# Optimization experiments

Measured on AMD Instinct MI355X. Metric: run time of the kernel, lower is better.

The kernel has to match this reference:

```python
import jax, jax.numpy as jnp
import numpy as np

LOCAL_K = 3
TOKEN_T, TOKEN_H, TOKEN_W = 8, 32, 32  # N = T*H*W = 8192
HIDDEN, N_HEADS = 256, 8


def _gather_neighbors(kv):
    # kv: [B, N, D2] -> [B, N, 27, D2] of 3x3x3 neighborhood (zero padded)
    B, N, D2 = kv.shape
    pad = LOCAL_K // 2
    x3d = kv.reshape(B, TOKEN_T, TOKEN_H, TOKEN_W, D2)
    x3d = jnp.pad(x3d, ((0, 0), (pad, pad), (pad, pad), (pad, pad), (0, 0)))
    slices = [
        x3d[:, dt:dt + TOKEN_T, dh:dh + TOKEN_H, dw:dw + TOKEN_W, :]
        for dt in range(LOCAL_K)
        for dh in range(LOCAL_K)
        for dw in range(LOCAL_K)
    ]
    nb = jnp.stack(slices, axis=4)  # [B, T, H, W, 27, D2]
    return nb.reshape(B, N, LOCAL_K ** 3, D2)


def setup_inputs() -> dict:
    key = jax.random.key(0)
    k1, k2, k3 = jax.random.split(key, 3)
    B, N, D = 2, TOKEN_T * TOKEN_H * TOKEN_W, HIDDEN
    x = jax.random.normal(k1, (B, N, D), dtype=jnp.float32)
    w_qkv = jax.random.normal(k2, (3 * D, D), dtype=jnp.float32) * (D ** -0.5)
    w_out = jax.random.normal(k3, (D, D), dtype=jnp.float32) * (D ** -0.5)
    return {"x": x, "w_qkv": w_qkv, "w_out": w_out}


def reference(x, w_qkv, w_out):
    B, N, D = x.shape
    H, d = N_HEADS, D // N_HEADS
    qkv = x @ w_qkv.T                       # [B, N, 3D]
    q, k, v = jnp.split(qkv, 3, axis=-1)
    kv_nb = _gather_neighbors(jnp.concatenate([k, v], axis=-1))  # [B,N,27,2D]
    k_nb, v_nb = jnp.split(kv_nb, 2, axis=-1)
    q = q.reshape(B, N, H, d)
    k_nb = k_nb.reshape(B, N, 27, H, d)
    v_nb = v_nb.reshape(B, N, 27, H, d)
    scale = 1.0 / jnp.sqrt(jnp.asarray(d, dtype=q.dtype))
    scores = jnp.einsum('bnhd,bnkhd->bnhk', q, k_nb) * scale  # [B,N,H,27]
    attn = jax.nn.softmax(scores, axis=-1)
    out = jnp.einsum('bnhk,bnkhd->bnhd', attn, v_nb)           # [B,N,H,d]
    return out.reshape(B, N, D) @ w_out.T
```

## Files before the change

kernel.cpp:

```cpp
#include <hip/hip_runtime.h>
#include <hip/hip_bf16.h>

#define TOK_T 8
#define TOK_H 32
#define TOK_W 32
#define NTOK 8192
#define BATCH 2
#define DMODEL 256
#define D3 768
#define NHEADS 8
#define DHEAD 32

using short8  = __attribute__((ext_vector_type(8))) short;
using ushort8 = __attribute__((ext_vector_type(8))) unsigned short;
using f32x4   = __attribute__((ext_vector_type(4))) float;
using f32x2   = __attribute__((ext_vector_type(2))) float;

__device__ __forceinline__ ushort f2bf(float f) {
  __hip_bfloat16 h = __float2bfloat16(f);
  return *reinterpret_cast<ushort*>(&h);
}
__device__ __forceinline__ float bf2f(ushort u) {
  union { unsigned u; float f; } v; v.u = ((unsigned)u) << 16;
  return v.f;
}
__device__ __forceinline__ f32x2 bfpair(unsigned u) {
  union { unsigned u; float f; } lo, hi;
  lo.u = u << 16;
  hi.u = u & 0xffff0000u;
  f32x2 r; r[0] = lo.f; r[1] = hi.f;
  return r;
}

template<int TBM, int TBN, int NW, int NBN, bool AF32, bool OUTBF16>
__global__ __launch_bounds__(NW * 64, 4) void gemm_fused(const void* __restrict__ Av,
                                                         const float* __restrict__ B,
                                                         void* __restrict__ Cv,
                                                         int ldc) {
  constexpr int NCW = TBN / 64;
  constexpr int NWR = NW / NCW;
  constexpr int MR  = TBM / (NWR * 16);
  constexpr int CHA = TBM * 4;
  constexpr int CHB = TBN * 4;
  constexpr int NT  = NW * 64;
  constexpr int CPT = (CHA + CHB) / NT;
  constexpr int SA  = CHA / NT;
  constexpr int ATILE = TBM * 32;
  constexpr int BTILE = TBN * 32;

  __shared__ __align__(16) ushort sm[2][ATILE + BTILE];

  const int tid  = threadIdx.x;
  const int lane = tid & 63;
  const int wid  = tid >> 6;
  const int wr   = wid / NCW;
  const int wc   = wid % NCW;
  const int bid  = blockIdx.x;
  const int xcd  = bid & 7;
  const int kk2  = bid >> 3;
  const int bm   = ((kk2 / NBN) * 8 + xcd) * TBM;
  const int bn   = (kk2 % NBN) * TBN;
  const int fr   = lane & 15;
  const int kb   = lane >> 4;

  float4  laf[SA > 0 ? SA : 1][2];
  ushort8 lab[SA > 0 ? SA : 1];
  float4  lbf[CPT - SA][2];

  auto load = [&](int kt) {
#pragma unroll
    for (int s = 0; s < SA; ++s) {
      int cc = tid + s * NT;
      int r = cc >> 2, sl = cc & 3;
      if constexpr (AF32) {
        const float* p = (const float*)Av + (size_t)(bm + r) * 256 + kt + sl * 8;
        laf[s][0] = *(const float4*)p;
        laf[s][1] = *(const float4*)(p + 4);
      } else {
        lab[s] = *(const ushort8*)((const ushort*)Av + (size_t)(bm + r) * 256 + kt + sl * 8);
      }
    }
#pragma unroll
    for (int s = 0; s < CPT - SA; ++s) {
      int cc = tid + (s + SA) * NT - CHA;
      int r = cc >> 2, sl = cc & 3;
      const float* p = B + (size_t)(bn + r) * 256 + kt + sl * 8;
      lbf[s][0] = *(const float4*)p;
      lbf[s][1] = *(const float4*)(p + 4);
    }
  };
  auto stow = [&](int buf) {
#pragma unroll
    for (int s = 0; s < SA; ++s) {
      int cc = tid + s * NT;
      int r = cc >> 2, sl = cc & 3;
      int sck = r * 4 + (sl ^ ((r >> 1) & 3));
      ushort8 v;
      if constexpr (AF32) {
        v[0] = f2bf(laf[s][0].x); v[1] = f2bf(laf[s][0].y);
        v[2] = f2bf(laf[s][0].z); v[3] = f2bf(laf[s][0].w);
        v[4] = f2bf(laf[s][1].x); v[5] = f2bf(laf[s][1].y);
        v[6] = f2bf(laf[s][1].z); v[7] = f2bf(laf[s][1].w);
      } else v = lab[s];
      *(ushort8*)&sm[buf][sck * 8] = v;
    }
#pragma unroll
    for (int s = 0; s < CPT - SA; ++s) {
      int cc = tid + (s + SA) * NT - CHA;
      int r = cc >> 2, sl = cc & 3;
      int sck = r * 4 + (sl ^ ((r >> 1) & 3));
      ushort8 v;
      v[0] = f2bf(lbf[s][0].x); v[1] = f2bf(lbf[s][0].y);
      v[2] = f2bf(lbf[s][0].z); v[3] = f2bf(lbf[s][0].w);
      v[4] = f2bf(lbf[s][1].x); v[5] = f2bf(lbf[s][1].y);
      v[6] = f2bf(lbf[s][1].z); v[7] = f2bf(lbf[s][1].w);
      *(ushort8*)&sm[buf][ATILE + sck * 8] = v;
    }
  };

  f32x4 acc[MR][4] = {};

  load(0);
  stow(0);
  __syncthreads();

  for (int it = 0; it < 8; ++it) {
    const int cur = it & 1;
    if (it < 7) load((it + 1) * 32);

    short8 af[MR], bf8[4];
#pragma unroll
    for (int m = 0; m < MR; ++m) {
      int r  = wr * (MR * 16) + m * 16 + fr;
      int ck = r * 4 + (kb ^ ((r >> 1) & 3));
      af[m] = *(const short8*)&sm[cur][ck * 8];
    }
#pragma unroll
    for (int n = 0; n < 4; ++n) {
      int r  = wc * 64 + n * 16 + fr;
      int ck = r * 4 + (kb ^ ((r >> 1) & 3));
      bf8[n] = *(const short8*)&sm[cur][ATILE + ck * 8];
    }
#pragma unroll
    for (int m = 0; m < MR; ++m)
#pragma unroll
      for (int n = 0; n < 4; ++n)
        acc[m][n] = __builtin_amdgcn_mfma_f32_16x16x32_bf16(af[m], bf8[n], acc[m][n], 0, 0, 0);

    if (it < 7) {
      stow(cur ^ 1);
      __syncthreads();
    }
  }

  if constexpr (OUTBF16) {
    ushort* C = (ushort*)Cv;
#pragma unroll
    for (int m = 0; m < MR; ++m)
#pragma unroll
      for (int n = 0; n < 4; ++n)
#pragma unroll
        for (int j = 0; j < 4; ++j) {
          int row = bm + wr * (MR * 16) + m * 16 + kb * 4 + j;
          int col = bn + wc * 64 + n * 16 + fr;
          C[(size_t)row * ldc + col] = f2bf(acc[m][n][j]);
        }
  } else {
    float* C = (float*)Cv;
#pragma unroll
    for (int m = 0; m < MR; ++m)
#pragma unroll
      for (int n = 0; n < 4; ++n)
#pragma unroll
        for (int j = 0; j < 4; ++j) {
          int row = bm + wr * (MR * 16) + m * 16 + kb * 4 + j;
          int col = bn + wc * 64 + n * 16 + fr;
          C[(size_t)row * ldc + col] = acc[m][n][j];
        }
  }
}

#define HALO 600

__global__ __launch_bounds__(256, 2) void local_attn(const ushort* __restrict__ qkv,
                                                     ushort* __restrict__ aob) {
  __shared__ __align__(16) ushort sh[HALO * 64];
  const int tile = blockIdx.x;
  const int head = blockIdx.y;
  const int b    = blockIdx.z;
  const int tz = tile >> 4;
  const int ty = (tile >> 2) & 3;
  const int tx = tile & 3;
  const int t0 = tz * 4, h0 = ty * 8, w0 = tx * 8;
  const int tid = threadIdx.x;

  for (int idx = tid; idx < HALO; idx += 256) {
    int ht  = idx / 100;
    int rem = idx - ht * 100;
    int hh  = rem / 10;
    int hw  = rem - hh * 10;
    int gt = t0 - 1 + ht, gh = h0 - 1 + hh, gw = w0 - 1 + hw;
    ushort* row = &sh[idx * 64];
    const int sw = idx & 7;
    if (gt >= 0 && gt < TOK_T && gh >= 0 && gh < TOK_H && gw >= 0 && gw < TOK_W) {
      size_t base = ((size_t)b * NTOK + (size_t)gt * 1024 + gh * 32 + gw) * D3;
      const ushort8* ks = (const ushort8*)(qkv + base + DMODEL + head * DHEAD);
      const ushort8* vs = (const ushort8*)(qkv + base + 2 * DMODEL + head * DHEAD);
#pragma unroll
      for (int p = 0; p < 4; ++p) *(ushort8*)&row[(p ^ sw) * 8]       = ks[p];
#pragma unroll
      for (int p = 0; p < 4; ++p) *(ushort8*)&row[((4 + p) ^ sw) * 8] = vs[p];
    } else {
      ushort8 z = (ushort8)0;
#pragma unroll
      for (int s = 0; s < 8; ++s) *(ushort8*)&row[s * 8] = z;
    }
  }

  const int tt = tid >> 6;
  const int th = (tid >> 3) & 7;
  const int tw = tid & 7;
  const int n  = (t0 + tt) * 1024 + (h0 + th) * 32 + (w0 + tw);

  const ushort* qp = qkv + ((size_t)b * NTOK + n) * D3 + head * DHEAD;
  f32x2 q2[16];
  {
    const ushort8* qs = (const ushort8*)qp;
#pragma unroll
    for (int p = 0; p < 4; ++p) {
      union { ushort8 s; uint4 u; } v; v.s = qs[p];
      q2[p * 4 + 0] = bfpair(v.u.x);
      q2[p * 4 + 1] = bfpair(v.u.y);
      q2[p * 4 + 2] = bfpair(v.u.z);
      q2[p * 4 + 3] = bfpair(v.u.w);
    }
  }
  __syncthreads();

  const float scale = 0.1767766952966369f;
  float s[27];
#pragma unroll
  for (int nb = 0; nb < 27; ++nb) {
    int dt = nb / 9, dh = (nb / 3) % 3, dw = nb % 3;
    int hidx = (tt + dt) * 100 + (th + dh) * 10 + (tw + dw);
    const ushort* row = &sh[hidx * 64];
    const int sw = hidx & 7;
    f32x2 a2 = {0.f, 0.f};
#pragma unroll
    for (int p = 0; p < 4; ++p) {
      union { ushort8 s; uint4 u; } kk; kk.s = *(const ushort8*)&row[(p ^ sw) * 8];
      a2 += q2[p * 4 + 0] * bfpair(kk.u.x);
      a2 += q2[p * 4 + 1] * bfpair(kk.u.y);
      a2 += q2[p * 4 + 2] * bfpair(kk.u.z);
      a2 += q2[p * 4 + 3] * bfpair(kk.u.w);
    }
    s[nb] = (a2[0] + a2[1]) * scale;
  }

  float mx = s[0];
#pragma unroll
  for (int nb = 1; nb < 27; ++nb) mx = fmaxf(mx, s[nb]);

  f32x2 o2[16] = {};
  float sum = 0.f;
#pragma unroll
  for (int nb = 0; nb < 27; ++nb) {
    int dt = nb / 9, dh = (nb / 3) % 3, dw = nb % 3;
    int hidx = (tt + dt) * 100 + (th + dh) * 10 + (tw + dw);
    const ushort* row = &sh[hidx * 64];
    const int sw = hidx & 7;
    float p = __expf(s[nb] - mx);
    sum += p;
    f32x2 p2; p2[0] = p; p2[1] = p;
#pragma unroll
    for (int c = 0; c < 4; ++c) {
      union { ushort8 s; uint4 u; } vv; vv.s = *(const ushort8*)&row[((4 + c) ^ sw) * 8];
      o2[c * 4 + 0] += p2 * bfpair(vv.u.x);
      o2[c * 4 + 1] += p2 * bfpair(vv.u.y);
      o2[c * 4 + 2] += p2 * bfpair(vv.u.z);
      o2[c * 4 + 3] += p2 * bfpair(vv.u.w);
    }
  }

  float inv = 1.f / sum;
  ushort8 os[4];
#pragma unroll
  for (int c = 0; c < 4; ++c)
#pragma unroll
    for (int e = 0; e < 8; ++e)
      os[c][e] = f2bf(o2[c * 4 + (e >> 1)][e & 1] * inv);
  ushort8* op = (ushort8*)(aob + ((size_t)b * NTOK + n) * DMODEL + head * DHEAD);
#pragma unroll
  for (int c = 0; c < 4; ++c) op[c] = os[c];
}

extern "C" void kernel_launch(void* const* d_in, const int* in_sizes, int n_in,
                              void* d_out, int out_size, void* d_ws, size_t ws_size,
                              hipStream_t stream) {
  const float* x     = (const float*)d_in[0];
  const float* w_qkv = (const float*)d_in[1];
  const float* w_out = (const float*)d_in[2];
  float* out = (float*)d_out;

  char* ws = (char*)d_ws;
  ushort* qkvb = (ushort*)ws;
  ushort* aob  = (ushort*)(ws + (size_t)BATCH * NTOK * D3 * 2);

  gemm_fused<128, 256, 8, 3, true, true><<<384, 512, 0, stream>>>(
      (const void*)x, w_qkv, (void*)qkvb, D3);

  local_attn<<<dim3(32, NHEADS, BATCH), 256, 0, stream>>>(qkvb, aob);

  gemm_fused<64, 128, 4, 2, false, false><<<512, 256, 0, stream>>>(
      (const void*)aob, w_out, (void*)out, DMODEL);
}
```

Baseline: 55.67 us.

## Stage K and V halos sequentially in half-size LDS to raise occupancy

```diff
diff --git a/kernel.cpp b/kernel.cpp
--- a/kernel.cpp
+++ b/kernel.cpp
@@ -182,9 +182,9 @@
 
 #define HALO 600
 
-__global__ __launch_bounds__(256, 2) void local_attn(const ushort* __restrict__ qkv,
+__global__ __launch_bounds__(256, 4) void local_attn(const ushort* __restrict__ qkv,
                                                      ushort* __restrict__ aob) {
-  __shared__ __align__(16) ushort sh[HALO * 64];
+  __shared__ __align__(16) ushort sh[HALO * 32];
   const int tile = blockIdx.x;
   const int head = blockIdx.y;
   const int b    = blockIdx.z;
@@ -194,28 +194,30 @@
   const int t0 = tz * 4, h0 = ty * 8, w0 = tx * 8;
   const int tid = threadIdx.x;
 
-  for (int idx = tid; idx < HALO; idx += 256) {
-    int ht  = idx / 100;
-    int rem = idx - ht * 100;
-    int hh  = rem / 10;
-    int hw  = rem - hh * 10;
-    int gt = t0 - 1 + ht, gh = h0 - 1 + hh, gw = w0 - 1 + hw;
-    ushort* row = &sh[idx * 64];
-    const int sw = idx & 7;
-    if (gt >= 0 && gt < TOK_T && gh >= 0 && gh < TOK_H && gw >= 0 && gw < TOK_W) {
-      size_t base = ((size_t)b * NTOK + (size_t)gt * 1024 + gh * 32 + gw) * D3;
-      const ushort8* ks = (const ushort8*)(qkv + base + DMODEL + head * DHEAD);
-      const ushort8* vs = (const ushort8*)(qkv + base + 2 * DMODEL + head * DHEAD);
-#pragma unroll
-      for (int p = 0; p < 4; ++p) *(ushort8*)&row[(p ^ sw) * 8]       = ks[p];
-#pragma unroll
-      for (int p = 0; p < 4; ++p) *(ushort8*)&row[((4 + p) ^ sw) * 8] = vs[p];
-    } else {
-      ushort8 z = (ushort8)0;
-#pragma unroll
-      for (int s = 0; s < 8; ++s) *(ushort8*)&row[s * 8] = z;
-    }
-  }
+  auto stage = [&](int ofs) {
+#pragma unroll
+    for (int k = 0; k < 10; ++k) {
+      int u = tid + k * 256;
+      if (u < HALO * 4) {
+        int row = u >> 2;
+        int q   = u & 3;
+        int ht  = row / 100;
+        int rem = row - ht * 100;
+        int hh  = rem / 10;
+        int hw  = rem - hh * 10;
+        int gt = t0 - 1 + ht, gh = h0 - 1 + hh, gw = w0 - 1 + hw;
+        uint4 v = {0u, 0u, 0u, 0u};
+        if (gt >= 0 && gt < TOK_T && gh >= 0 && gh < TOK_H && gw >= 0 && gw < TOK_W) {
+          size_t base = ((size_t)b * NTOK + (size_t)gt * 1024 + gh * 32 + gw) * D3
+                        + ofs + head * DHEAD + q * 8;
+          v = *(const uint4*)(qkv + base);
+        }
+        *(uint4*)&sh[row * 32 + ((q ^ (row & 3)) * 8)] = v;
+      }
+    }
+  };
+
+  stage(DMODEL);
 
   const int tt = tid >> 6;
   const int th = (tid >> 3) & 7;
@@ -243,8 +245,8 @@
   for (int nb = 0; nb < 27; ++nb) {
     int dt = nb / 9, dh = (nb / 3) % 3, dw = nb % 3;
     int hidx = (tt + dt) * 100 + (th + dh) * 10 + (tw + dw);
-    const ushort* row = &sh[hidx * 64];
-    const int sw = hidx & 7;
+    const ushort* row = &sh[hidx * 32];
+    const int sw = hidx & 3;
     f32x2 a2 = {0.f, 0.f};
 #pragma unroll
     for (int p = 0; p < 4; ++p) {
@@ -256,10 +258,14 @@
     }
     s[nb] = (a2[0] + a2[1]) * scale;
   }
+  __syncthreads();
+
+  stage(2 * DMODEL);
 
   float mx = s[0];
 #pragma unroll
   for (int nb = 1; nb < 27; ++nb) mx = fmaxf(mx, s[nb]);
+  __syncthreads();
 
   f32x2 o2[16] = {};
   float sum = 0.f;
@@ -267,14 +273,14 @@
   for (int nb = 0; nb < 27; ++nb) {
     int dt = nb / 9, dh = (nb / 3) % 3, dw = nb % 3;
     int hidx = (tt + dt) * 100 + (th + dh) * 10 + (tw + dw);
-    const ushort* row = &sh[hidx * 64];
-    const int sw = hidx & 7;
+    const ushort* row = &sh[hidx * 32];
+    const int sw = hidx & 3;
     float p = __expf(s[nb] - mx);
     sum += p;
     f32x2 p2; p2[0] = p; p2[1] = p;
 #pragma unroll
     for (int c = 0; c < 4; ++c) {
-      union { ushort8 s; uint4 u; } vv; vv.s = *(const ushort8*)&row[((4 + c) ^ sw) * 8];
+      union { ushort8 s; uint4 u; } vv; vv.s = *(const ushort8*)&row[(c ^ sw) * 8];
       o2[c * 4 + 0] += p2 * bfpair(vv.u.x);
       o2[c * 4 + 1] += p2 * bfpair(vv.u.y);
       o2[c * 4 + 2] += p2 * bfpair(vv.u.z);
```

Result: slower. 206.0 us (+270.1%).
